# Optimization experiments

Hardware: AMD Instinct MI355X
Metric: run time of the kernel (lower is better)

## Reference

```python
import jax, jax.numpy as jnp
import numpy as np

BETA, GAMMA, ZETA = 0.66, -0.1, 1.1  # hard-concrete params
N, E, S = 20000, 640000, 256          # nodes, edges, samples (node feature dim)
D, P, PH, OUT = 2000, 500, 100, 2     # DEmRNA, pathway, pathway-hidden, out nodes


def setup_inputs() -> dict:
    key = jax.random.key(0)
    ks = jax.random.split(key, 14)
    return {
        "lnc_data": jax.random.normal(ks[0], (S, 8000), jnp.float32),
        "mi_data": jax.random.normal(ks[1], (S, 2000), jnp.float32),
        "m_data": jax.random.normal(ks[2], (S, 10000), jnp.float32),
        "src": jax.random.randint(ks[3], (E,), 0, N, dtype=jnp.int32),
        "dst": jax.random.randint(ks[4], (E,), 0, N, dtype=jnp.int32),
        "demrna_index": jax.random.randint(ks[5], (D,), 0, N, dtype=jnp.int32),
        "attn_l": jax.random.normal(ks[6], (N, 1), jnp.float32) * 0.01,
        "attn_r": jax.random.normal(ks[7], (N, 1), jnp.float32) * 0.01,
        "bias_l0": jnp.zeros((1,), jnp.float32),
        "pathway_mask": (jax.random.uniform(ks[8], (P, D)) < 0.1).astype(jnp.float32),
        "W_mp": jax.random.normal(ks[9], (P, D), jnp.float32) * (1.414 / np.sqrt(D)),
        "b_mp": jnp.zeros((P,), jnp.float32),
        "W_ph": jax.random.normal(ks[10], (PH, P), jnp.float32) * 0.05,
        "b_ph": jnp.zeros((PH,), jnp.float32),
        "W_po": jax.random.normal(ks[11], (OUT, PH), jnp.float32) * 0.1,
        "b_po": jnp.zeros((OUT,), jnp.float32),
    }


def _standardize(x):
    # torch pre_process: per-column (dim 0) mean/std, std unbiased (ddof=1)
    return (x - x.mean(axis=0)) / x.std(axis=0, ddof=1)


def reference(lnc_data, mi_data, m_data, src, dst, demrna_index,
              attn_l, attn_r, bias_l0, pathway_mask,
              W_mp, b_mp, W_ph, b_ph, W_po, b_po):
    rna = jnp.concatenate([lnc_data, mi_data, m_data], axis=1)  # [S, N]
    a_rna = _standardize(rna.T)                                  # [N, S] node feats

    # per-node attention logits (attn_l/r broadcast over sample dim)
    a1 = (a_rna * attn_l).sum(-1, keepdims=True)                 # [N, 1]
    a2 = (a_rna * attn_r).sum(-1, keepdims=True)                 # [N, 1]

    # edge attention with hard-concrete L0 gate (eval / l0_test path)
    logits = a1[src] + a2[dst] + bias_l0                         # [E, 1]
    s = jax.nn.sigmoid(logits / BETA)
    a = jnp.clip(s * (ZETA - GAMMA) + GAMMA, 0.0, 1.0)

    # custom edge-softmax: normalize by per-dst sum of gates
    z = jax.ops.segment_sum(a, dst, num_segments=N)              # [N, 1]
    a = a / z[dst]
    a = jnp.where(jnp.isnan(a), 0.0, a)                          # 0/0 -> 0

    # two rounds of u_mul_e + sum scatter aggregation
    rna1 = jax.ops.segment_sum(a * a_rna[src], dst, num_segments=N)  # [N, S]
    rna2 = jax.ops.segment_sum(a * rna1[src], dst, num_segments=N)   # [N, S]

    x = (a_rna + rna1 + rna2).T[:, demrna_index]                 # [S, D]

    # pas_net pathway branch (weight masked by pathway_mask each forward)
    h = jax.nn.relu(x @ (W_mp * pathway_mask).T + b_mp)          # [S, P]
    h = jax.nn.relu(h @ W_ph.T + b_ph)                           # [S, PH]
    return jax.nn.softmax(h @ W_po.T + b_po, axis=1)             # [S, OUT]
```

## Files before the change

### kernel.cpp

```cpp
#include <hip/hip_runtime.h>

#define NN 20000
#define EE 640000
#define SS 256
#define DD 2000
#define PP 500
#define PHH 100
#define ZSPLIT 25
#define KCH 80
#define SUB 10

typedef unsigned short ushort_t;

__device__ __forceinline__ unsigned short f2bf(float f) {
  unsigned u = __float_as_uint(f);
  unsigned r = (u + 0x7FFFu + ((u >> 16) & 1u)) >> 16;
  return (unsigned short)r;
}
__device__ __forceinline__ float lo16(unsigned u) { return __uint_as_float(u << 16); }
__device__ __forceinline__ float hi16(unsigned u) { return __uint_as_float(u & 0xFFFF0000u); }

__global__ __launch_bounds__(256) void k_pre(
    const float* __restrict__ lnc, const float* __restrict__ mi,
    const float* __restrict__ mdat, float* __restrict__ mean,
    float* __restrict__ invstd, const float* __restrict__ Wmp,
    const float* __restrict__ pmask, float* __restrict__ Wt,
    int* __restrict__ counts) {
  int b = blockIdx.x;
  int tx = threadIdx.x, ty = threadIdx.y;
  int tid = ty * 32 + tx;
  if (b < 256) {
    int s = b;
    double sum = 0.0, ssq = 0.0;
    const float4* L = (const float4*)(lnc + (size_t)s * 8000);
    const float4* M = (const float4*)(mi + (size_t)s * 2000);
    const float4* D = (const float4*)(mdat + (size_t)s * 10000);
    for (int i = tid; i < 2000; i += 256) {
      float4 v = L[i];
      sum += (double)v.x + (double)v.y + (double)v.z + (double)v.w;
      ssq += (double)v.x * v.x + (double)v.y * v.y + (double)v.z * v.z + (double)v.w * v.w;
    }
    for (int i = tid; i < 500; i += 256) {
      float4 v = M[i];
      sum += (double)v.x + (double)v.y + (double)v.z + (double)v.w;
      ssq += (double)v.x * v.x + (double)v.y * v.y + (double)v.z * v.z + (double)v.w * v.w;
    }
    for (int i = tid; i < 2500; i += 256) {
      float4 v = D[i];
      sum += (double)v.x + (double)v.y + (double)v.z + (double)v.w;
      ssq += (double)v.x * v.x + (double)v.y * v.y + (double)v.z * v.z + (double)v.w * v.w;
    }
    __shared__ double sm[256], sq[256];
    sm[tid] = sum; sq[tid] = ssq; __syncthreads();
    for (int o = 128; o > 0; o >>= 1) {
      if (tid < o) { sm[tid] += sm[tid + o]; sq[tid] += sq[tid + o]; }
      __syncthreads();
    }
    if (tid == 0) {
      double mu = sm[0] / 20000.0;
      double var = (sq[0] - 20000.0 * mu * mu) / 19999.0;
      mean[s] = (float)mu;
      invstd[s] = (float)(1.0 / sqrt(var));
    }
  } else if (b < 1264) {
    __shared__ float tile[32][33];
    int b2 = b - 256;
    int p0 = (b2 & 15) * 32, d0 = (b2 >> 4) * 32;
    for (int r = ty; r < 32; r += 8) {
      int p = p0 + r, d = d0 + tx;
      float v = 0.f;
      if (p < PP && d < DD) v = Wmp[(size_t)p * DD + d] * pmask[(size_t)p * DD + d];
      tile[r][tx] = v;
    }
    __syncthreads();
    for (int r = ty; r < 32; r += 8) {
      int d = d0 + r, p = p0 + tx;
      if (d < DD) Wt[(size_t)d * 512 + p] = tile[tx][r];
    }
  } else {
    int idx = (b - 1264) * 256 + tid;
    if (idx < NN / 4) {
      uint4 z; z.x = 0; z.y = 0; z.z = 0; z.w = 0;
      ((uint4*)counts)[idx] = z;
    }
  }
}

__global__ __launch_bounds__(256) void k_prep(
    const float* __restrict__ lnc, const float* __restrict__ mi,
    const float* __restrict__ mdat, const float* __restrict__ mean,
    const float* __restrict__ invstd, ushort_t* __restrict__ a_rna,
    float* __restrict__ rowsum4, const int* __restrict__ dst,
    int* __restrict__ counts) {
  int b = blockIdx.x;
  int tx = threadIdx.x, ty = threadIdx.y;
  if (b < 2500) {
    __shared__ float tile[64][33];
    __shared__ float red[8][33];
    int nb = (b % 625) * 32, sb = (b / 625) * 64;
    int n = nb + tx;
    const float* base; int w, c;
    if (n < 8000)       { base = lnc;  w = 8000;  c = n; }
    else if (n < 10000) { base = mi;   w = 2000;  c = n - 8000; }
    else                { base = mdat; w = 10000; c = n - 10000; }
    for (int r = ty; r < 64; r += 8) {
      int s = sb + r;
      tile[r][tx] = (base[(size_t)s * w + c] - mean[s]) * invstd[s];
    }
    __syncthreads();
    float ps = 0.f;
    for (int r = ty; r < 64; r += 8) ps += tile[r][tx];
    red[ty][tx] = ps;
    __syncthreads();
    if (ty == 0) {
      float t = 0.f;
      #pragma unroll
      for (int j = 0; j < 8; ++j) t += red[j][tx];
      rowsum4[(size_t)(sb >> 6) * NN + nb + tx] = t;
    }
    ushort2* out2 = (ushort2*)a_rna;
    for (int r2 = ty; r2 < 32; r2 += 8) {
      int nn = nb + r2;
      ushort2 v;
      v.x = f2bf(tile[2 * tx][r2]);
      v.y = f2bf(tile[2 * tx + 1][r2]);
      out2[(size_t)nn * 128 + (sb >> 1) + tx] = v;
    }
  } else {
    int e = (b - 2500) * 256 + ty * 32 + tx;
    if (e < EE) atomicAdd(&counts[dst[e]], 1);
  }
}

__global__ __launch_bounds__(1024) void k_scan(
    const int* __restrict__ counts, int* __restrict__ offsets, int* __restrict__ cursor,
    const float* __restrict__ rowsum4, const float* __restrict__ attnl,
    const float* __restrict__ attnr, float* __restrict__ a1, float* __restrict__ a2) {
  if (blockIdx.x == 0) {
    __shared__ int sums[1024];
    int t = threadIdx.x;
    int base = t * 20;
    int local[20];
    int s = 0;
    for (int i = 0; i < 20; ++i) {
      int idx = base + i;
      int c = (idx < NN) ? counts[idx] : 0;
      local[i] = s; s += c;
    }
    sums[t] = s; __syncthreads();
    for (int d = 1; d < 1024; d <<= 1) {
      int v = (t >= d) ? sums[t - d] : 0;
      __syncthreads();
      sums[t] += v;
      __syncthreads();
    }
    int prefix = (t > 0) ? sums[t - 1] : 0;
    for (int i = 0; i < 20; ++i) {
      int idx = base + i;
      if (idx < NN) { int o = prefix + local[i]; offsets[idx] = o; cursor[idx] = o; }
    }
    if (t == 1023) offsets[NN] = sums[1023];
  } else {
    int n = (blockIdx.x - 1) * 1024 + threadIdx.x;
    if (n < NN) {
      float t = rowsum4[n] + rowsum4[NN + n] + rowsum4[2 * NN + n] + rowsum4[3 * NN + n];
      a1[n] = attnl[n] * t;
      a2[n] = attnr[n] * t;
    }
  }
}

__device__ __forceinline__ float hc_gate(float l) {
  float sg = 1.0f / (1.0f + __expf(-l * 1.5151515151f));
  return fminf(fmaxf(fmaf(sg, 1.2f, -0.1f), 0.0f), 1.0f);
}

__global__ __launch_bounds__(256) void k_fill(
    const int* __restrict__ src, const int* __restrict__ dst,
    const float* __restrict__ a1, const float* __restrict__ a2,
    const float* __restrict__ bias0, int* __restrict__ cursor,
    uint2* __restrict__ csr) {
  int e = blockIdx.x * 256 + threadIdx.x;
  if (e >= EE) return;
  int d = dst[e], s = src[e];
  float a = hc_gate(a1[s] + a2[d] + bias0[0]);
  int slot = atomicAdd(&cursor[d], 1);
  uint2 rec; rec.x = (unsigned)s; rec.y = __float_as_uint(a);
  csr[slot] = rec;
}

__global__ __launch_bounds__(256) void k_agg(
    const uint2* __restrict__ csr, const int* __restrict__ offs,
    const ushort_t* __restrict__ in_bf, ushort_t* __restrict__ out_bf,
    float* __restrict__ zinv) {
  int wave = threadIdx.x >> 6, lane = threadIdx.x & 63;
  int half = lane >> 5, sl = lane & 31;
  int n = blockIdx.x * 4 + wave;
  int beg = __builtin_amdgcn_readfirstlane(offs[n]);
  int end = __builtin_amdgcn_readfirstlane(offs[n + 1]);

  const uint4* in4 = (const uint4*)in_bf;
  float acc[8] = {0.f, 0.f, 0.f, 0.f, 0.f, 0.f, 0.f, 0.f};
  float zsum = 0.f;
  int i = beg;
  for (; i + 15 < end; i += 16) {
    uint2 r[8]; uint4 v[8];
    #pragma unroll
    for (int j = 0; j < 8; ++j) r[j] = csr[i + 2 * j + half];
    #pragma unroll
    for (int j = 0; j < 8; ++j) v[j] = in4[(size_t)r[j].x * 32 + sl];
    #pragma unroll
    for (int j = 0; j < 8; ++j) {
      float g = __uint_as_float(r[j].y);
      zsum += g;
      acc[0] += g * lo16(v[j].x); acc[1] += g * hi16(v[j].x);
      acc[2] += g * lo16(v[j].y); acc[3] += g * hi16(v[j].y);
      acc[4] += g * lo16(v[j].z); acc[5] += g * hi16(v[j].z);
      acc[6] += g * lo16(v[j].w); acc[7] += g * hi16(v[j].w);
    }
  }
  for (; i + 3 < end; i += 4) {
    uint2 rA = csr[i + half];
    uint2 rB = csr[i + 2 + half];
    uint4 vA = in4[(size_t)rA.x * 32 + sl];
    uint4 vB = in4[(size_t)rB.x * 32 + sl];
    float gA = __uint_as_float(rA.y), gB = __uint_as_float(rB.y);
    zsum += gA + gB;
    acc[0] += gA * lo16(vA.x) + gB * lo16(vB.x);
    acc[1] += gA * hi16(vA.x) + gB * hi16(vB.x);
    acc[2] += gA * lo16(vA.y) + gB * lo16(vB.y);
    acc[3] += gA * hi16(vA.y) + gB * hi16(vB.y);
    acc[4] += gA * lo16(vA.z) + gB * lo16(vB.z);
    acc[5] += gA * hi16(vA.z) + gB * hi16(vB.z);
    acc[6] += gA * lo16(vA.w) + gB * lo16(vB.w);
    acc[7] += gA * hi16(vA.w) + gB * hi16(vB.w);
  }
  for (; i + 1 < end; i += 2) {
    uint2 rA = csr[i + half];
    uint4 vA = in4[(size_t)rA.x * 32 + sl];
    float gA = __uint_as_float(rA.y);
    zsum += gA;
    acc[0] += gA * lo16(vA.x); acc[1] += gA * hi16(vA.x);
    acc[2] += gA * lo16(vA.y); acc[3] += gA * hi16(vA.y);
    acc[4] += gA * lo16(vA.z); acc[5] += gA * hi16(vA.z);
    acc[6] += gA * lo16(vA.w); acc[7] += gA * hi16(vA.w);
  }
  if (i < end && half == 0) {
    uint2 rA = csr[i];
    uint4 vA = in4[(size_t)rA.x * 32 + sl];
    float gA = __uint_as_float(rA.y);
    zsum += gA;
    acc[0] += gA * lo16(vA.x); acc[1] += gA * hi16(vA.x);
    acc[2] += gA * lo16(vA.y); acc[3] += gA * hi16(vA.y);
    acc[4] += gA * lo16(vA.z); acc[5] += gA * hi16(vA.z);
    acc[6] += gA * lo16(vA.w); acc[7] += gA * hi16(vA.w);
  }
  #pragma unroll
  for (int j = 0; j < 8; ++j) acc[j] += __shfl_xor(acc[j], 32, 64);
  float z = zsum + __shfl_xor(zsum, 32, 64);
  float inv = (z > 0.f) ? 1.0f / z : 0.0f;
  if (lane == 0) zinv[n] = inv;
  if (half == 0) {
    uint4 w;
    w.x = (unsigned)f2bf(acc[0] * inv) | ((unsigned)f2bf(acc[1] * inv) << 16);
    w.y = (unsigned)f2bf(acc[2] * inv) | ((unsigned)f2bf(acc[3] * inv) << 16);
    w.z = (unsigned)f2bf(acc[4] * inv) | ((unsigned)f2bf(acc[5] * inv) << 16);
    w.w = (unsigned)f2bf(acc[6] * inv) | ((unsigned)f2bf(acc[7] * inv) << 16);
    ((uint4*)out_bf)[(size_t)n * 32 + sl] = w;
  }
}

__global__ __launch_bounds__(256) void k_pass2x(
    const int* __restrict__ dem, const int* __restrict__ offs,
    const uint2* __restrict__ csr, const ushort_t* __restrict__ a_rna,
    const ushort_t* __restrict__ rna1, const float* __restrict__ zinv,
    float* __restrict__ xt) {
  int wave = threadIdx.x >> 6, lane = threadIdx.x & 63;
  int half = lane >> 5, sl = lane & 31;
  int d = blockIdx.x * 4 + wave;
  int nd = dem[d];
  const uint4* ar = (const uint4*)a_rna;
  const uint4* r1 = (const uint4*)rna1;
  int beg = __builtin_amdgcn_readfirstlane(offs[nd]);
  int end = __builtin_amdgcn_readfirstlane(offs[nd + 1]);
  float inv = zinv[nd];
  float acc[8] = {0.f, 0.f, 0.f, 0.f, 0.f, 0.f, 0.f, 0.f};
  int i = beg;
  for (; i + 3 < end; i += 4) {
    uint2 rA = csr[i + half];
    uint2 rB = csr[i + 2 + half];
    uint4 vA = r1[(size_t)rA.x * 32 + sl];
    uint4 vB = r1[(size_t)rB.x * 32 + sl];
    float gA = __uint_as_float(rA.y) * inv, gB = __uint_as_float(rB.y) * inv;
    acc[0] += gA * lo16(vA.x) + gB * lo16(vB.x);
    acc[1] += gA * hi16(vA.x) + gB * hi16(vB.x);
    acc[2] += gA * lo16(vA.y) + gB * lo16(vB.y);
    acc[3] += gA * hi16(vA.y) + gB * hi16(vB.y);
    acc[4] += gA * lo16(vA.z) + gB * lo16(vB.z);
    acc[5] += gA * hi16(vA.z) + gB * hi16(vB.z);
    acc[6] += gA * lo16(vA.w) + gB * lo16(vB.w);
    acc[7] += gA * hi16(vA.w) + gB * hi16(vB.w);
  }
  for (; i + 1 < end; i += 2) {
    uint2 rA = csr[i + half];
    uint4 vA = r1[(size_t)rA.x * 32 + sl];
    float gA = __uint_as_float(rA.y) * inv;
    acc[0] += gA * lo16(vA.x); acc[1] += gA * hi16(vA.x);
    acc[2] += gA * lo16(vA.y); acc[3] += gA * hi16(vA.y);
    acc[4] += gA * lo16(vA.z); acc[5] += gA * hi16(vA.z);
    acc[6] += gA * lo16(vA.w); acc[7] += gA * hi16(vA.w);
  }
  if (i < end && half == 0) {
    uint2 rA = csr[i];
    uint4 vA = r1[(size_t)rA.x * 32 + sl];
    float gA = __uint_as_float(rA.y) * inv;
    acc[0] += gA * lo16(vA.x); acc[1] += gA * hi16(vA.x);
    acc[2] += gA * lo16(vA.y); acc[3] += gA * hi16(vA.y);
    acc[4] += gA * lo16(vA.z); acc[5] += gA * hi16(vA.z);
    acc[6] += gA * lo16(vA.w); acc[7] += gA * hi16(vA.w);
  }
  #pragma unroll
  for (int j = 0; j < 8; ++j) acc[j] += __shfl_xor(acc[j], 32, 64);
  if (half == 0) {
    uint4 va = ar[(size_t)nd * 32 + sl];
    uint4 vb = r1[(size_t)nd * 32 + sl];
    acc[0] += lo16(va.x) + lo16(vb.x); acc[1] += hi16(va.x) + hi16(vb.x);
    acc[2] += lo16(va.y) + lo16(vb.y); acc[3] += hi16(va.y) + hi16(vb.y);
    acc[4] += lo16(va.z) + lo16(vb.z); acc[5] += hi16(va.z) + hi16(vb.z);
    acc[6] += lo16(va.w) + lo16(vb.w); acc[7] += hi16(va.w) + hi16(vb.w);
    float4* xo = (float4*)&xt[(size_t)d * SS + sl * 8];
    float4 w0; w0.x = acc[0]; w0.y = acc[1]; w0.z = acc[2]; w0.w = acc[3];
    float4 w1; w1.x = acc[4]; w1.y = acc[5]; w1.z = acc[6]; w1.w = acc[7];
    xo[0] = w0; xo[1] = w1;
  }
}

__global__ __launch_bounds__(256) void k_gemm1(
    const float* __restrict__ xt, const float* __restrict__ Wt,
    float* __restrict__ partial) {
  __shared__ float As[SUB][64];
  __shared__ float Ws[SUB][68];
  int tid = threadIdx.x;
  int s0 = blockIdx.x * 64, p0 = blockIdx.y * 64, d0 = blockIdx.z * KCH;
  int ts = tid & 15, tp = tid >> 4;
  float acc[4][4];
  #pragma unroll
  for (int i = 0; i < 4; ++i)
    #pragma unroll
    for (int j = 0; j < 4; ++j) acc[i][j] = 0.f;

  for (int kt = 0; kt < KCH / SUB; ++kt) {
    int dd = d0 + kt * SUB;
    #pragma unroll
    for (int i = tid; i < SUB * 64; i += 256) {
      int r = i >> 6, c = i & 63;
      As[r][c] = xt[(size_t)(dd + r) * SS + s0 + c];
    }
    #pragma unroll
    for (int i = tid; i < SUB * 64; i += 256) {
      int r = i >> 6, c = i & 63;
      Ws[r][c] = Wt[(size_t)(dd + r) * 512 + p0 + c];
    }
    __syncthreads();
    #pragma unroll
    for (int kk = 0; kk < SUB; ++kk) {
      float4 a = *(const float4*)&As[kk][ts * 4];
      float4 b = *(const float4*)&Ws[kk][tp * 4];
      acc[0][0] += a.x * b.x; acc[0][1] += a.x * b.y; acc[0][2] += a.x * b.z; acc[0][3] += a.x * b.w;
      acc[1][0] += a.y * b.x; acc[1][1] += a.y * b.y; acc[1][2] += a.y * b.z; acc[1][3] += a.y * b.w;
      acc[2][0] += a.z * b.x; acc[2][1] += a.z * b.y; acc[2][2] += a.z * b.z; acc[2][3] += a.z * b.w;
      acc[3][0] += a.w * b.x; acc[3][1] += a.w * b.y; acc[3][2] += a.w * b.z; acc[3][3] += a.w * b.w;
    }
    __syncthreads();
  }
  float* dstp = partial + (size_t)blockIdx.z * 512 * 256;
  #pragma unroll
  for (int j = 0; j < 4; ++j) {
    int p = p0 + tp * 4 + j;
    float4 w; w.x = acc[0][j]; w.y = acc[1][j]; w.z = acc[2][j]; w.w = acc[3][j];
    *(float4*)&dstp[(size_t)p * 256 + s0 + ts * 4] = w;
  }
}

__global__ __launch_bounds__(256) void k_reduce(
    const float* __restrict__ partial, const float* __restrict__ bmp,
    float* __restrict__ h1t) {
  int idx4 = blockIdx.x * 256 + threadIdx.x;
  if (idx4 >= PP * SS / 4) return;
  int p = idx4 >> 6;
  float b = bmp[p];
  float4 acc; acc.x = b; acc.y = b; acc.z = b; acc.w = b;
  #pragma unroll
  for (int z = 0; z < ZSPLIT; ++z) {
    float4 v = ((const float4*)partial)[(size_t)z * 512 * 64 + idx4];
    acc.x += v.x; acc.y += v.y; acc.z += v.z; acc.w += v.w;
  }
  acc.x = fmaxf(acc.x, 0.f); acc.y = fmaxf(acc.y, 0.f);
  acc.z = fmaxf(acc.z, 0.f); acc.w = fmaxf(acc.w, 0.f);
  ((float4*)h1t)[idx4] = acc;
}

__global__ __launch_bounds__(64) void k_h2(
    const float* __restrict__ h1t, const float* __restrict__ Wph,
    const float* __restrict__ bph, float* __restrict__ h2t) {
  int ph = blockIdx.x;
  int s = blockIdx.y * 64 + threadIdx.x;
  const float* w = &Wph[(size_t)ph * PP];
  float acc[10];
  #pragma unroll
  for (int j = 0; j < 10; ++j) acc[j] = 0.f;
  for (int k = 0; k < 50; ++k) {
    int p = k * 10;
    #pragma unroll
    for (int j = 0; j < 10; ++j)
      acc[j] = fmaf(h1t[(size_t)(p + j) * SS + s], w[p + j], acc[j]);
  }
  float t = ((acc[0] + acc[1]) + (acc[2] + acc[3])) + ((acc[4] + acc[5]) + (acc[6] + acc[7])) + (acc[8] + acc[9]);
  h2t[(size_t)ph * SS + s] = fmaxf(t + bph[ph], 0.0f);
}

__global__ __launch_bounds__(256) void k_out(
    const float* __restrict__ h2t, const float* __restrict__ Wpo,
    const float* __restrict__ bpo, float* __restrict__ out) {
  int s = threadIdx.x;
  float o0 = bpo[0], o1 = bpo[1];
  for (int ph = 0; ph < PHH; ++ph) {
    float v = h2t[(size_t)ph * SS + s];
    o0 += v * Wpo[ph];
    o1 += v * Wpo[PHH + ph];
  }
  float mx = fmaxf(o0, o1);
  float e0 = __expf(o0 - mx), e1 = __expf(o1 - mx);
  float inv = 1.0f / (e0 + e1);
  out[2 * s] = e0 * inv;
  out[2 * s + 1] = e1 * inv;
}

extern "C" void kernel_launch(void* const* d_in, const int* in_sizes, int n_in,
                              void* d_out, int out_size, void* d_ws, size_t ws_size,
                              hipStream_t stream) {
  const float* lnc   = (const float*)d_in[0];
  const float* mi    = (const float*)d_in[1];
  const float* mdat  = (const float*)d_in[2];
  const int*   src   = (const int*)d_in[3];
  const int*   dst   = (const int*)d_in[4];
  const int*   dem   = (const int*)d_in[5];
  const float* attnl = (const float*)d_in[6];
  const float* attnr = (const float*)d_in[7];
  const float* bias0 = (const float*)d_in[8];
  const float* pmask = (const float*)d_in[9];
  const float* Wmp   = (const float*)d_in[10];
  const float* bmp   = (const float*)d_in[11];
  const float* Wph   = (const float*)d_in[12];
  const float* bph   = (const float*)d_in[13];
  const float* Wpo   = (const float*)d_in[14];
  const float* bpo   = (const float*)d_in[15];
  float* out = (float*)d_out;

  char* ws = (char*)d_ws;
  size_t off = 0;
  auto alloc = [&](size_t bytes) -> char* {
    char* p = ws + off;
    off += (bytes + 255) & ~(size_t)255;
    return p;
  };
  float*    mean    = (float*)alloc(SS * 4);
  float*    invstd  = (float*)alloc(SS * 4);
  float*    a1      = (float*)alloc(NN * 4);
  float*    a2      = (float*)alloc(NN * 4);
  float*    rowsum4 = (float*)alloc((size_t)4 * NN * 4);
  float*    zinv    = (float*)alloc(NN * 4);
  int*      counts  = (int*)alloc(NN * 4);
  int*      offs    = (int*)alloc((NN + 1) * 4);
  int*      cursor  = (int*)alloc(NN * 4);
  uint2*    csr     = (uint2*)alloc((size_t)EE * 8);
  ushort_t* a_rna   = (ushort_t*)alloc((size_t)NN * SS * 2);
  ushort_t* rna1    = (ushort_t*)alloc((size_t)NN * SS * 2);
  float*    xt      = (float*)alloc((size_t)DD * SS * 4);
  float*    Wt      = (float*)alloc((size_t)DD * 512 * 4);
  float*    partial = (float*)alloc((size_t)ZSPLIT * 512 * 256 * 4);
  float*    h1t     = (float*)alloc((size_t)PP * SS * 4);
  float*    h2t     = (float*)alloc((size_t)PHH * SS * 4);

  k_pre<<<1284, dim3(32, 8), 0, stream>>>(lnc, mi, mdat, mean, invstd, Wmp, pmask, Wt, counts);
  k_prep<<<5000, dim3(32, 8), 0, stream>>>(lnc, mi, mdat, mean, invstd, a_rna, rowsum4, dst, counts);
  k_scan<<<21, 1024, 0, stream>>>(counts, offs, cursor, rowsum4, attnl, attnr, a1, a2);
  k_fill<<<(EE + 255) / 256, 256, 0, stream>>>(src, dst, a1, a2, bias0, cursor, csr);
  k_agg<<<NN / 4, 256, 0, stream>>>(csr, offs, a_rna, rna1, zinv);
  k_pass2x<<<DD / 4, 256, 0, stream>>>(dem, offs, csr, a_rna, rna1, zinv, xt);
  k_gemm1<<<dim3(SS / 64, 8, ZSPLIT), 256, 0, stream>>>(xt, Wt, partial);
  k_reduce<<<(PP * SS / 4 + 255) / 256, 256, 0, stream>>>(partial, bmp, h1t);
  k_h2<<<dim3(PHH, SS / 64), 64, 0, stream>>>(h1t, Wph, bph, h2t);
  k_out<<<1, SS, 0, stream>>>(h2t, Wpo, bpo, out);
}
```

Baseline: 198.6 us.

## Split k_agg feature columns across grid.y and process eight edges per wave

The aggregation kernel now splits the 256-sample row into four column slices via a second grid dimension. Each wave handles 8 edges at once in groups of 8 lanes, each lane loading 16 bytes of a 128-byte slice, and reduces across groups with three shuffles. This raises parallelism and memory-level concurrency on the gather, since there are 4x more waves and more edges in flight per wave. The cost is that the CSR records are read four times and the loads per row become smaller 128-byte segments.

```diff
diff --git a/kernel.cpp b/kernel.cpp
--- a/kernel.cpp
+++ b/kernel.cpp
@@ -194,36 +194,20 @@
     const ushort_t* __restrict__ in_bf, ushort_t* __restrict__ out_bf,
     float* __restrict__ zinv) {
   int wave = threadIdx.x >> 6, lane = threadIdx.x & 63;
-  int half = lane >> 5, sl = lane & 31;
+  int grp = lane >> 3, q = lane & 7;
   int n = blockIdx.x * 4 + wave;
+  int colbase = blockIdx.y * 8 + q;
   int beg = __builtin_amdgcn_readfirstlane(offs[n]);
   int end = __builtin_amdgcn_readfirstlane(offs[n + 1]);
-
   const uint4* in4 = (const uint4*)in_bf;
   float acc[8] = {0.f, 0.f, 0.f, 0.f, 0.f, 0.f, 0.f, 0.f};
   float zsum = 0.f;
   int i = beg;
   for (; i + 15 < end; i += 16) {
-    uint2 r[8]; uint4 v[8];
-    #pragma unroll
-    for (int j = 0; j < 8; ++j) r[j] = csr[i + 2 * j + half];
-    #pragma unroll
-    for (int j = 0; j < 8; ++j) v[j] = in4[(size_t)r[j].x * 32 + sl];
-    #pragma unroll
-    for (int j = 0; j < 8; ++j) {
-      float g = __uint_as_float(r[j].y);
-      zsum += g;
-      acc[0] += g * lo16(v[j].x); acc[1] += g * hi16(v[j].x);
-      acc[2] += g * lo16(v[j].y); acc[3] += g * hi16(v[j].y);
-      acc[4] += g * lo16(v[j].z); acc[5] += g * hi16(v[j].z);
-      acc[6] += g * lo16(v[j].w); acc[7] += g * hi16(v[j].w);
-    }
-  }
-  for (; i + 3 < end; i += 4) {
-    uint2 rA = csr[i + half];
-    uint2 rB = csr[i + 2 + half];
-    uint4 vA = in4[(size_t)rA.x * 32 + sl];
-    uint4 vB = in4[(size_t)rB.x * 32 + sl];
+    uint2 rA = csr[i + grp];
+    uint2 rB = csr[i + 8 + grp];
+    uint4 vA = in4[(size_t)rA.x * 32 + colbase];
+    uint4 vB = in4[(size_t)rB.x * 32 + colbase];
     float gA = __uint_as_float(rA.y), gB = __uint_as_float(rB.y);
     zsum += gA + gB;
     acc[0] += gA * lo16(vA.x) + gB * lo16(vB.x);
@@ -235,9 +219,9 @@
     acc[6] += gA * lo16(vA.w) + gB * lo16(vB.w);
     acc[7] += gA * hi16(vA.w) + gB * hi16(vB.w);
   }
-  for (; i + 1 < end; i += 2) {
-    uint2 rA = csr[i + half];
-    uint4 vA = in4[(size_t)rA.x * 32 + sl];
+  for (; i + 7 < end; i += 8) {
+    uint2 rA = csr[i + grp];
+    uint4 vA = in4[(size_t)rA.x * 32 + colbase];
     float gA = __uint_as_float(rA.y);
     zsum += gA;
     acc[0] += gA * lo16(vA.x); acc[1] += gA * hi16(vA.x);
@@ -245,9 +229,9 @@
     acc[4] += gA * lo16(vA.z); acc[5] += gA * hi16(vA.z);
     acc[6] += gA * lo16(vA.w); acc[7] += gA * hi16(vA.w);
   }
-  if (i < end && half == 0) {
-    uint2 rA = csr[i];
-    uint4 vA = in4[(size_t)rA.x * 32 + sl];
+  if (i + grp < end) {
+    uint2 rA = csr[i + grp];
+    uint4 vA = in4[(size_t)rA.x * 32 + colbase];
     float gA = __uint_as_float(rA.y);
     zsum += gA;
     acc[0] += gA * lo16(vA.x); acc[1] += gA * hi16(vA.x);
@@ -256,17 +240,23 @@
     acc[6] += gA * lo16(vA.w); acc[7] += gA * hi16(vA.w);
   }
   #pragma unroll
-  for (int j = 0; j < 8; ++j) acc[j] += __shfl_xor(acc[j], 32, 64);
-  float z = zsum + __shfl_xor(zsum, 32, 64);
-  float inv = (z > 0.f) ? 1.0f / z : 0.0f;
-  if (lane == 0) zinv[n] = inv;
-  if (half == 0) {
+  for (int j = 0; j < 8; ++j) {
+    acc[j] += __shfl_xor(acc[j], 8, 64);
+    acc[j] += __shfl_xor(acc[j], 16, 64);
+    acc[j] += __shfl_xor(acc[j], 32, 64);
+  }
+  zsum += __shfl_xor(zsum, 8, 64);
+  zsum += __shfl_xor(zsum, 16, 64);
+  zsum += __shfl_xor(zsum, 32, 64);
+  float inv = (zsum > 0.f) ? 1.0f / zsum : 0.0f;
+  if (blockIdx.y == 0 && lane == 0) zinv[n] = inv;
+  if (grp == 0) {
     uint4 w;
     w.x = (unsigned)f2bf(acc[0] * inv) | ((unsigned)f2bf(acc[1] * inv) << 16);
     w.y = (unsigned)f2bf(acc[2] * inv) | ((unsigned)f2bf(acc[3] * inv) << 16);
     w.z = (unsigned)f2bf(acc[4] * inv) | ((unsigned)f2bf(acc[5] * inv) << 16);
     w.w = (unsigned)f2bf(acc[6] * inv) | ((unsigned)f2bf(acc[7] * inv) << 16);
-    ((uint4*)out_bf)[(size_t)n * 32 + sl] = w;
+    ((uint4*)out_bf)[(size_t)n * 32 + colbase] = w;
   }
 }
 
@@ -486,7 +476,7 @@
   k_prep<<<5000, dim3(32, 8), 0, stream>>>(lnc, mi, mdat, mean, invstd, a_rna, rowsum4, dst, counts);
   k_scan<<<21, 1024, 0, stream>>>(counts, offs, cursor, rowsum4, attnl, attnr, a1, a2);
   k_fill<<<(EE + 255) / 256, 256, 0, stream>>>(src, dst, a1, a2, bias0, cursor, csr);
-  k_agg<<<NN / 4, 256, 0, stream>>>(csr, offs, a_rna, rna1, zinv);
+  k_agg<<<dim3(NN / 4, 4), 256, 0, stream>>>(csr, offs, a_rna, rna1, zinv);
   k_pass2x<<<DD / 4, 256, 0, stream>>>(dem, offs, csr, a_rna, rna1, zinv, xt);
   k_gemm1<<<dim3(SS / 64, 8, ZSPLIT), 256, 0, stream>>>(xt, Wt, partial);
   k_reduce<<<(PP * SS / 4 + 255) / 256, 256, 0, stream>>>(partial, bmp, h1t);
```

New measurement: 203.6 us. 2.5% more time.
